# Optimization experiments

Hardware: AMD Instinct MI355X
Metric: run time of the kernel (lower is better)

The kernel has to match this reference:

```python
import jax, jax.numpy as jnp
import numpy as np

ALPHA = 0.2  # LeakyReLU slope
EPS = 1e-5   # LayerNorm eps (torch default)
NEG = -9e15  # pyGAT mask fill


def _lnorm(x, g, b):
    mu = x.mean(-1, keepdims=True)
    var = ((x - mu) ** 2).mean(-1, keepdims=True)
    return (x - mu) / jnp.sqrt(var + EPS) * g + b


def _gat_rel(h, adj, W, a1, a2):
    # Canonical dense GAT layer, vectorized over relations.
    # h [N,di], adj [R,N,N] int, W [R,di,do], a1/a2 [R,do]
    Wh = jnp.einsum('ni,rio->rno', h, W)                     # [R,N,do]
    f1 = jnp.einsum('rno,ro->rn', Wh, a1)
    f2 = jnp.einsum('rno,ro->rn', Wh, a2)
    e = jax.nn.leaky_relu(f1[:, :, None] + f2[:, None, :], ALPHA)  # [R,N,N]
    att = jax.nn.softmax(jnp.where(adj > 0, e, NEG), axis=-1)
    return jax.nn.elu(jnp.einsum('rnm,rmo->rno', att, Wh))   # [R,N,do]


def setup_inputs() -> dict:
    key = jax.random.key(0)
    N, D, R, Q, C = 2048, 512, 4, 32, 64
    HE, HD = 2, 2
    ks = jax.random.split(key, 16)
    s = 0.05
    return {
        'x': jax.random.normal(ks[0], (N, D), jnp.float32),
        'rel_adj': jax.random.randint(ks[1], (R, N, N), 0, 2, jnp.int32),
        'qembedding1': jax.random.normal(ks[2], (Q, D), jnp.float32),
        'qnode_idx': jax.random.randint(ks[3], (8,), 0, N, jnp.int32),
        'choices_nodes_idx': jax.random.randint(ks[4], (5, C), 0, N, jnp.int32),
        'Wc': jax.random.normal(ks[5], (D, D), jnp.float32) * s,
        'bc': jnp.zeros((D,), jnp.float32),
        'wq': jax.random.normal(ks[6], (D,), jnp.float32) * s,
        'enc_W': jax.random.normal(ks[7], (HE, R, D, D), jnp.float32) * s,
        'enc_a1': jax.random.normal(ks[8], (HE, R, D), jnp.float32) * s,
        'enc_a2': jax.random.normal(ks[9], (HE, R, D), jnp.float32) * s,
        'dec_W': jax.random.normal(ks[10], (HD, R, D, D), jnp.float32) * s,
        'dec_a1': jax.random.normal(ks[11], (HD, R, D), jnp.float32) * s,
        'dec_a2': jax.random.normal(ks[12], (HD, R, D), jnp.float32) * s,
        'ln_g': jnp.ones((D,), jnp.float32),
        'ln_b': jnp.zeros((D,), jnp.float32),
        'Wqc': jax.random.normal(ks[13], (D, D), jnp.float32) * s,
        'bqc': jnp.zeros((D,), jnp.float32),
        'Wout': jax.random.normal(ks[14], (D, 1), jnp.float32) * s,
        'bout': jnp.zeros((1,), jnp.float32),
    }


def reference(x, rel_adj, qembedding1, qnode_idx, choices_nodes_idx,
              Wc, bc, wq, enc_W, enc_a1, enc_a2, dec_W, dec_a1, dec_a2,
              ln_g, ln_b, Wqc, bqc, Wout, bout):
    # QuestionLayer: attention-pool the question token sequence -> [D]
    qemb = jax.nn.softmax(qembedding1 @ wq) @ qembedding1
    # question-gated node embeddings (Conv1d k=1 == linear over features)
    p = jax.nn.sigmoid((x @ Wc.T + bc) @ qemb)[:, None]       # [N,1]
    x = p * x + (1.0 - p) * qemb[None, :]
    # encoder: per-relation GAT + LayerNorm, maxpool over relations
    for h in range(enc_W.shape[0]):
        xr = _gat_rel(x, rel_adj, enc_W[h], enc_a1[h], enc_a2[h])
        x = _lnorm(xr, ln_g, ln_b).max(axis=0)                # [N,D]
    # decoder (transpose attentions): last round skips LayerNorm
    xd = x
    HD = dec_W.shape[0]
    for i in range(HD):
        xr = _gat_rel(xd, rel_adj, dec_W[i], dec_a1[i], dec_a2[i])
        if i < HD - 1:
            xr = _lnorm(xr, ln_g, ln_b)
        xd = xr.max(axis=0)
    # QuestionChoiceLayer over the 5 choices (all present -> mask gate = 1)
    cnodes = x[choices_nodes_idx]                             # [5,C,D]
    qproj = qembedding1.mean(axis=0) @ Wqc + bqc              # [D]
    scores = jax.nn.softmax(jnp.einsum('kcd,d->kc', cnodes, qproj), axis=-1)
    cembed = jnp.einsum('kc,kcd->kd', scores, cnodes)         # [5,D]
    cout = jax.nn.log_softmax(cembed @ Wout + bout, axis=0)   # [5,1]
    return cout, xd
```

## Files before the change

kernel.cpp:

```cpp
#include <hip/hip_runtime.h>
#include <hip/hip_bf16.h>

typedef __hip_bfloat16 bf16;
typedef __attribute__((ext_vector_type(8))) short bf16x8_t;
typedef __attribute__((ext_vector_type(4))) float f32x4_t;

#define N 2048
#define D 512
#define R 4
#define Q 32
#define NC 64
#define ALPHA 0.2f
#define LNEPS 1e-5f
#define NEGC -9e15f

__device__ __forceinline__ float ldf(const float* p) { return *p; }
__device__ __forceinline__ float ldf(const bf16* p) { return __bfloat162float(*p); }
__device__ __forceinline__ void stf(float* p, float v) { *p = v; }
__device__ __forceinline__ void stf(bf16* p, float v) { *p = __float2bfloat16(v); }

__device__ __forceinline__ short f2b(float f) {
    unsigned u = __builtin_bit_cast(unsigned, f);
    unsigned r = u + 0x7FFFu + ((u >> 16) & 1u);
    return (short)(r >> 16);
}
__device__ __forceinline__ float b2fs(short s) {
    unsigned u = ((unsigned)(unsigned short)s) << 16;
    return __builtin_bit_cast(float, u);
}
__device__ __forceinline__ unsigned pk2(float a, float b) {
    return (unsigned)(unsigned short)f2b(a) | (((unsigned)(unsigned short)f2b(b)) << 16);
}

__device__ __forceinline__ float waveReduceSum(float v) {
#pragma unroll
    for (int o = 32; o > 0; o >>= 1) v += __shfl_down(v, o, 64);
    return v;
}
__device__ __forceinline__ float waveReduceMax(float v) {
#pragma unroll
    for (int o = 32; o > 0; o >>= 1) v = fmaxf(v, __shfl_down(v, o, 64));
    return v;
}

__global__ __launch_bounds__(512) void k_prep(const float* __restrict__ qe1, const float* __restrict__ wq,
                                              const float* __restrict__ Wc, const float* __restrict__ bc,
                                              const float* __restrict__ Wqc, const float* __restrict__ bqc,
                                              float* __restrict__ qemb, float* __restrict__ vvec,
                                              float* __restrict__ qproj, float* __restrict__ c0) {
    __shared__ float logits[Q];
    __shared__ float sw[Q];
    __shared__ float meanq[D];
    __shared__ float qembs[D];
    __shared__ float red8[8];
    int tid = threadIdx.x;
    int wave = tid >> 6, lane = tid & 63;
    for (int q = wave; q < Q; q += 8) {
        float s = 0.f;
        for (int d = lane; d < D; d += 64) s += qe1[q * D + d] * wq[d];
        s = waveReduceSum(s);
        if (lane == 0) logits[q] = s;
    }
    __syncthreads();
    if (tid == 0) {
        float m = -3e38f;
        for (int q = 0; q < Q; q++) m = fmaxf(m, logits[q]);
        float ssum = 0.f;
        for (int q = 0; q < Q; q++) { float e = __expf(logits[q] - m); sw[q] = e; ssum += e; }
        float inv = 1.f / ssum;
        for (int q = 0; q < Q; q++) sw[q] *= inv;
    }
    __syncthreads();
    {
        float acc = 0.f, mq = 0.f;
#pragma unroll 4
        for (int q = 0; q < Q; q++) { float xv = qe1[q * D + tid]; acc += sw[q] * xv; mq += xv; }
        qembs[tid] = acc;
        meanq[tid] = mq * (1.f / Q);
        qemb[tid] = acc;
    }
    __syncthreads();
    {
        float v = 0.f, qp = 0.f;
        for (int i = 0; i < D; i++) {
            v = fmaf(qembs[i], Wc[i * D + tid], v);
            qp = fmaf(meanq[i], Wqc[i * D + tid], qp);
        }
        vvec[tid] = v;
        qproj[tid] = qp + bqc[tid];
    }
    float cc = qembs[tid] * bc[tid];
    cc = waveReduceSum(cc);
    if (lane == 0) red8[wave] = cc;
    __syncthreads();
    if (tid == 0) {
        float t = 0.f;
        for (int i = 0; i < 8; i++) t += red8[i];
        c0[0] = t;
    }
}

__global__ __launch_bounds__(256) void k_prepw(const float* __restrict__ W, short* __restrict__ Wt) {
    int mi = blockIdx.z;
    int k0 = blockIdx.y * 32, d0 = blockIdx.x * 32;
    __shared__ float L[32][33];
    int tid = threadIdx.x;
    const float* Wm = W + (size_t)mi * D * D;
    {
        int kr = tid >> 3, dc = (tid & 7) * 4;
        float4 f = *(const float4*)&Wm[(size_t)(k0 + kr) * D + d0 + dc];
        L[kr][dc] = f.x; L[kr][dc + 1] = f.y; L[kr][dc + 2] = f.z; L[kr][dc + 3] = f.w;
    }
    __syncthreads();
    short* Wo = Wt + (size_t)mi * D * D;
    {
        int dr = tid >> 3, kc = (tid & 7) * 4;
        uint2 o;
        o.x = pk2(L[kc][dr], L[kc + 1][dr]);
        o.y = pk2(L[kc + 2][dr], L[kc + 3][dr]);
        *(uint2*)&Wo[(size_t)(d0 + dr) * D + k0 + kc] = o;
    }
}

__global__ __launch_bounds__(256) void k_zero12(float* __restrict__ f1, float* __restrict__ f2) {
    int i = blockIdx.x * 256 + threadIdx.x;
    f1[i] = 0.f;
    f2[i] = 0.f;
}

__global__ __launch_bounds__(256) void k_gate(const float* __restrict__ x, const float* __restrict__ vvec,
                                              const float* __restrict__ qemb, const float* __restrict__ c0,
                                              bf16* __restrict__ xcur) {
    int n = blockIdx.x;
    int tid = threadIdx.x;
    __shared__ float red[4];
    __shared__ float ps;
    float x0 = x[n * D + tid], x1 = x[n * D + tid + 256];
    float v = x0 * vvec[tid] + x1 * vvec[tid + 256];
    v = waveReduceSum(v);
    if ((tid & 63) == 0) red[tid >> 6] = v;
    __syncthreads();
    if (tid == 0) {
        float dot = (red[0] + red[1]) + (red[2] + red[3]) + c0[0];
        ps = 1.f / (1.f + __expf(-dot));
    }
    __syncthreads();
    float p = ps;
    stf(&xcur[n * D + tid], p * x0 + (1.f - p) * qemb[tid]);
    stf(&xcur[n * D + tid + 256], p * x1 + (1.f - p) * qemb[tid + 256]);
}

__global__ __launch_bounds__(256) void k_gemm_mfma(const bf16* __restrict__ xin, const short* __restrict__ Wt,
                                                   short* __restrict__ WhT, const float* __restrict__ a1b,
                                                   const float* __restrict__ a2b, float* __restrict__ f1,
                                                   float* __restrict__ f2) {
    int r = blockIdx.z;
    int m0 = blockIdx.x * 64;
    int d0 = blockIdx.y * 64;
    int tid = threadIdx.x;
    int w = tid >> 6, l = tid & 63, g = l >> 4, rs = l & 15;
    int wn = w >> 1, wd = w & 1;
    __shared__ __align__(16) short Al[64 * 40];
    __shared__ __align__(16) short Bl[64 * 40];
    __shared__ __align__(16) short Tt[64 * 80];
    __shared__ float a1s[64], a2s[64];
    __shared__ float r1[4][64], r2[4][64];
    if (tid < 64) {
        a1s[tid] = a1b[r * D + d0 + tid];
        a2s[tid] = a2b[r * D + d0 + tid];
    }
    f32x4_t acc[2][2];
#pragma unroll
    for (int i = 0; i < 2; i++)
#pragma unroll
        for (int j = 0; j < 2; j++) acc[i][j] = (f32x4_t)(0.0f);

    const short* Wtr = Wt + (size_t)r * D * D;
    int sn = tid >> 2;
    int sk = (tid & 3) * 8;
    for (int k0 = 0; k0 < D; k0 += 32) {
        __syncthreads();
        {
            *(uint4*)&Al[sn * 40 + sk] = *(const uint4*)&xin[(size_t)(m0 + sn) * D + k0 + sk];
            *(uint4*)&Bl[sn * 40 + sk] = *(const uint4*)&Wtr[(size_t)(d0 + sn) * D + k0 + sk];
        }
        __syncthreads();
        union UA { bf16x8_t v; uint2 u[2]; };
        UA a[2], b;
#pragma unroll
        for (int nf = 0; nf < 2; nf++) {
            int arow = wn * 32 + nf * 16 + rs;
            a[nf].u[0] = *(const uint2*)&Al[arow * 40 + 4 * g];
            a[nf].u[1] = *(const uint2*)&Al[arow * 40 + 16 + 4 * g];
        }
#pragma unroll
        for (int df = 0; df < 2; df++) {
            int brow = wd * 32 + df * 16 + rs;
            b.u[0] = *(const uint2*)&Bl[brow * 40 + 4 * g];
            b.u[1] = *(const uint2*)&Bl[brow * 40 + 16 + 4 * g];
            acc[0][df] = __builtin_amdgcn_mfma_f32_16x16x32_bf16(a[0].v, b.v, acc[0][df], 0, 0, 0);
            acc[1][df] = __builtin_amdgcn_mfma_f32_16x16x32_bf16(a[1].v, b.v, acc[1][df], 0, 0, 0);
        }
    }
    __syncthreads();
#pragma unroll
    for (int nf = 0; nf < 2; nf++)
#pragma unroll
        for (int df = 0; df < 2; df++) {
            int nl = wn * 32 + nf * 16 + 4 * g;
            int dl = wd * 32 + df * 16 + rs;
            uint2 o;
            o.x = pk2(acc[nf][df][0], acc[nf][df][1]);
            o.y = pk2(acc[nf][df][2], acc[nf][df][3]);
            *(uint2*)&Tt[dl * 80 + nl] = o;
        }
    __syncthreads();
    {
        int dl = tid >> 2;
        int nc = (tid & 3) * 16;
        uint4 v0 = *(const uint4*)&Tt[dl * 80 + nc];
        uint4 v1 = *(const uint4*)&Tt[dl * 80 + nc + 8];
        short* op = WhT + ((size_t)r * D + d0 + dl) * N + m0 + nc;
        *(uint4*)op = v0;
        *(uint4*)(op + 8) = v1;
    }
    {
        int m = tid & 63, dg = tid >> 6;
        float s1 = 0.f, s2 = 0.f;
#pragma unroll
        for (int d = 0; d < 16; d++) {
            int dd = dg + d * 4;
            float wv = b2fs(Tt[dd * 80 + m]);
            s1 = fmaf(wv, a1s[dd], s1);
            s2 = fmaf(wv, a2s[dd], s2);
        }
        r1[dg][m] = s1;
        r2[dg][m] = s2;
    }
    __syncthreads();
    if (tid < 64) {
        float v1 = (r1[0][tid] + r1[1][tid]) + (r1[2][tid] + r1[3][tid]);
        float v2 = (r2[0][tid] + r2[1][tid]) + (r2[2][tid] + r2[3][tid]);
        atomicAdd(&f1[r * N + m0 + tid], v1);
        atomicAdd(&f2[r * N + m0 + tid], v2);
    }
}

__global__ __launch_bounds__(512) void k_pv_nm(const int* __restrict__ adj, const float* __restrict__ f1,
                                               const float* __restrict__ f2, const short* __restrict__ WhT,
                                               bf16* __restrict__ xr) {
    int r = blockIdx.y;
    int n0 = blockIdx.x * 32;
    int tid = threadIdx.x;
    int w = tid >> 6, l = tid & 63, g = l >> 4, rs = l & 15;
    __shared__ __align__(16) short Pl[2][32 * 40];
    __shared__ __align__(16) short Whl[2][512 * 40];
    __shared__ float sl[32], f1s[32];
    if (tid < 32) f1s[tid] = f1[r * N + n0 + tid];
    __syncthreads();
    f32x4_t acc[2][4];
#pragma unroll
    for (int i = 0; i < 2; i++)
#pragma unroll
        for (int j = 0; j < 4; j++) acc[i][j] = (f32x4_t)(0.0f);

    int pn = tid >> 3, pm4 = (tid & 7) * 4;
    const float* f2r = f2 + r * N;
    const int* arowb = adj + ((size_t)r * N + n0 + (pn & 31)) * N + pm4;
    int4 av;
    float4 fv;
    float f1v = 0.f;
    float myl = 0.f;
    int j = tid - 256;
    if (tid < 256) {
        f1v = f1s[pn];
        av = *(const int4*)(arowb);
        fv = *(const float4*)&f2r[pm4];
    }

    const int NT = N / 32;

#define PRODUCE(tt, bb)                                                                              \
    if (tid < 256) {                                                                                 \
        float t0 = f1v + fv.x; t0 = t0 >= 0.f ? t0 : ALPHA * t0;                                     \
        float t1 = f1v + fv.y; t1 = t1 >= 0.f ? t1 : ALPHA * t1;                                     \
        float t2 = f1v + fv.z; t2 = t2 >= 0.f ? t2 : ALPHA * t2;                                     \
        float t3 = f1v + fv.w; t3 = t3 >= 0.f ? t3 : ALPHA * t3;                                     \
        float e0 = (av.x > 0) ? __expf(fminf(t0, 60.f)) : 0.f;                                       \
        float e1 = (av.y > 0) ? __expf(fminf(t1, 60.f)) : 0.f;                                       \
        float e2 = (av.z > 0) ? __expf(fminf(t2, 60.f)) : 0.f;                                       \
        float e3 = (av.w > 0) ? __expf(fminf(t3, 60.f)) : 0.f;                                       \
        myl += (e0 + e1) + (e2 + e3);                                                                \
        uint2 pw;                                                                                    \
        pw.x = pk2(e0, e1);                                                                          \
        pw.y = pk2(e2, e3);                                                                          \
        *(uint2*)&Pl[bb][pn * 40 + pm4] = pw;                                                        \
        if ((tt) + 1 < NT) {                                                                         \
            av = *(const int4*)(arowb + ((tt) + 1) * 32);                                            \
            fv = *(const float4*)&f2r[((tt) + 1) * 32 + pm4];                                        \
        }                                                                                            \
    } else {                                                                                         \
        _Pragma("unroll") for (int i = 0; i < 8; i++) {                                              \
            int v = j + i * 256;                                                                     \
            int dd = v >> 2, mc = (v & 3) * 8;                                                       \
            *(uint4*)&Whl[bb][dd * 40 + mc] = *(const uint4*)&WhT[((size_t)r * D + dd) * N + (tt) * 32 + mc]; \
        }                                                                                            \
    }

    PRODUCE(0, 0);
    __syncthreads();

    for (int t = 0; t < NT; t++) {
        int cur = t & 1;
        if (t + 1 < NT) { PRODUCE(t + 1, (cur ^ 1)); }
        union UA { bf16x8_t v; uint2 u[2]; };
        UA a[2], b;
#pragma unroll
        for (int nf = 0; nf < 2; nf++) {
            int arow = nf * 16 + rs;
            a[nf].u[0] = *(const uint2*)&Pl[cur][arow * 40 + 4 * g];
            a[nf].u[1] = *(const uint2*)&Pl[cur][arow * 40 + 16 + 4 * g];
        }
#pragma unroll
        for (int df = 0; df < 4; df++) {
            int brow = w * 64 + df * 16 + rs;
            b.u[0] = *(const uint2*)&Whl[cur][brow * 40 + 4 * g];
            b.u[1] = *(const uint2*)&Whl[cur][brow * 40 + 16 + 4 * g];
            acc[0][df] = __builtin_amdgcn_mfma_f32_16x16x32_bf16(a[0].v, b.v, acc[0][df], 0, 0, 0);
            acc[1][df] = __builtin_amdgcn_mfma_f32_16x16x32_bf16(a[1].v, b.v, acc[1][df], 0, 0, 0);
        }
        __syncthreads();
    }
#undef PRODUCE
    if (tid < 256) {
        float v = myl;
#pragma unroll
        for (int msk = 1; msk < 8; msk <<= 1) v += __shfl_xor(v, msk, 8);
        if ((tid & 7) == 0) sl[pn] = v;
    }
    __syncthreads();
    float inv[2][4];
#pragma unroll
    for (int nf = 0; nf < 2; nf++)
#pragma unroll
        for (int reg = 0; reg < 4; reg++) inv[nf][reg] = 1.f / sl[nf * 16 + 4 * g + reg];
#pragma unroll
    for (int nf = 0; nf < 2; nf++)
#pragma unroll
        for (int df = 0; df < 4; df++)
#pragma unroll
            for (int reg = 0; reg < 4; reg++) {
                int n = n0 + nf * 16 + 4 * g + reg;
                int d = w * 64 + df * 16 + rs;
                float v = acc[nf][df][reg] * inv[nf][reg];
                v = v > 0.f ? v : (__expf(v) - 1.f);
                stf(&xr[((size_t)r * N + n) * D + d], v);
            }
}

__global__ __launch_bounds__(256) void k_lnmax(const bf16* __restrict__ xr, const float* __restrict__ g,
                                               const float* __restrict__ b, bf16* __restrict__ xout) {
    int n = blockIdx.x;
    int tid = threadIdx.x;
    int wave = tid >> 6, lane = tid & 63;
    __shared__ float redA[4], redB[4];
    float g0 = g[tid], g1 = g[tid + 256];
    float bb0 = b[tid], bb1 = b[tid + 256];
    float mx0 = -3e38f, mx1 = -3e38f;
    for (int r = 0; r < R; r++) {
        const bf16* row = xr + ((size_t)(r * N + n)) * D;
        float v0 = ldf(&row[tid]), v1 = ldf(&row[tid + 256]);
        float s = v0 + v1;
        float ss = fmaf(v0, v0, v1 * v1);
        s = waveReduceSum(s);
        ss = waveReduceSum(ss);
        if (lane == 0) { redA[wave] = s; redB[wave] = ss; }
        __syncthreads();
        float mu = ((redA[0] + redA[1]) + (redA[2] + redA[3])) * (1.f / D);
        float ex2 = ((redB[0] + redB[1]) + (redB[2] + redB[3])) * (1.f / D);
        float inv = 1.f / sqrtf(ex2 - mu * mu + LNEPS);
        mx0 = fmaxf(mx0, (v0 - mu) * inv * g0 + bb0);
        mx1 = fmaxf(mx1, (v1 - mu) * inv * g1 + bb1);
        __syncthreads();
    }
    stf(&xout[n * D + tid], mx0);
    stf(&xout[n * D + tid + 256], mx1);
}

__global__ __launch_bounds__(256) void k_maxout(const bf16* __restrict__ xr, float* __restrict__ out) {
    size_t idx = (size_t)blockIdx.x * 256 + threadIdx.x;
    float m = ldf(&xr[idx]);
    m = fmaxf(m, ldf(&xr[(size_t)N * D + idx]));
    m = fmaxf(m, ldf(&xr[2 * (size_t)N * D + idx]));
    m = fmaxf(m, ldf(&xr[3 * (size_t)N * D + idx]));
    out[idx] = m;
}

__global__ __launch_bounds__(256) void k_cscore(const bf16* __restrict__ xe, const int* __restrict__ cidx,
                                                const float* __restrict__ qproj, const float* __restrict__ Wout,
                                                float* __restrict__ scw, float* __restrict__ dvw) {
    int wv = threadIdx.x >> 6, lane = threadIdx.x & 63;
    int p = blockIdx.x * 4 + wv;
    const bf16* row = xe + (size_t)cidx[p] * D;
    float s1 = 0.f, s2 = 0.f;
#pragma unroll
    for (int i = 0; i < 8; i++) {
        int d = lane + i * 64;
        float v = ldf(&row[d]);
        s1 = fmaf(v, qproj[d], s1);
        s2 = fmaf(v, Wout[d], s2);
    }
    s1 = waveReduceSum(s1);
    s2 = waveReduceSum(s2);
    if (lane == 0) { scw[p] = s1; dvw[p] = s2; }
}

__global__ __launch_bounds__(64) void k_cfinal(const float* __restrict__ scw, const float* __restrict__ dvw,
                                               const float* __restrict__ bout, float* __restrict__ out) {
    int lane = threadIdx.x;
    __shared__ float lg[5];
    for (int k = 0; k < 5; k++) {
        float v = scw[k * NC + lane];
        float m = waveReduceMax(v);
        m = __shfl(m, 0, 64);
        float e = __expf(v - m);
        float s = waveReduceSum(e);
        s = __shfl(s, 0, 64);
        float t = (e / s) * dvw[k * NC + lane];
        t = waveReduceSum(t);
        if (lane == 0) lg[k] = t + bout[0];
    }
    __syncthreads();
    if (lane == 0) {
        float m = -3e38f;
        for (int k = 0; k < 5; k++) m = fmaxf(m, lg[k]);
        float s = 0.f;
        for (int k = 0; k < 5; k++) s += __expf(lg[k] - m);
        float lse = logf(s) + m;
        for (int k = 0; k < 5; k++) out[k] = lg[k] - lse;
    }
}

extern "C" void kernel_launch(void* const* d_in, const int* in_sizes, int n_in,
                              void* d_out, int out_size, void* d_ws, size_t ws_size,
                              hipStream_t stream) {
    bool skipQ = false;
    if (n_in > 4 && in_sizes[4] != 5 * NC && in_sizes[3] == 5 * NC) skipQ = true;
    auto IN = [&](int i) -> const void* {
        int j = (skipQ && i >= 4) ? i - 1 : i;
        return d_in[j];
    };
    const float* x = (const float*)IN(0);
    const int* adj = (const int*)IN(1);
    const float* qe1 = (const float*)IN(2);
    const int* cidx = (const int*)IN(4);
    const float* Wc = (const float*)IN(5);
    const float* bc = (const float*)IN(6);
    const float* wq = (const float*)IN(7);
    const float* encW = (const float*)IN(8);
    const float* enca1 = (const float*)IN(9);
    const float* enca2 = (const float*)IN(10);
    const float* decW = (const float*)IN(11);
    const float* deca1 = (const float*)IN(12);
    const float* deca2 = (const float*)IN(13);
    const float* lng = (const float*)IN(14);
    const float* lnb = (const float*)IN(15);
    const float* Wqc = (const float*)IN(16);
    const float* bqc = (const float*)IN(17);
    const float* Wout = (const float*)IN(18);
    const float* bout = (const float*)IN(19);
    float* out = (float*)d_out;

    char* w8 = (char*)d_ws;
    float* qemb = (float*)(w8 + 0);
    float* vvec = (float*)(w8 + 2048);
    float* qproj = (float*)(w8 + 4096);
    float* c0 = (float*)(w8 + 6144);
    float* f1 = (float*)(w8 + 8192);
    float* f2 = (float*)(w8 + 8192 + 32768);
    float* scw = (float*)(w8 + 8192 + 65536);
    float* dvw = (float*)(w8 + 8192 + 98304);
    const size_t ND = (size_t)N * D;
    bf16* xcur = (bf16*)(w8 + 139264);
    bf16* xd = (bf16*)(w8 + 139264 + ND * 2);
    short* WhT = (short*)(w8 + 139264 + ND * 4);
    bf16* xr = (bf16*)(w8 + 139264 + ND * 4 + R * ND * 2);
    short* Wt = (short*)xr;

    k_prep<<<1, 512, 0, stream>>>(qe1, wq, Wc, bc, Wqc, bqc, qemb, vvec, qproj, c0);
    k_gate<<<N, 256, 0, stream>>>(x, vvec, qemb, c0, xcur);

    for (int L = 0; L < 4; L++) {
        const float* Wb = (L < 2) ? encW + (size_t)L * R * D * D : decW + (size_t)(L - 2) * R * D * D;
        const float* a1 = (L < 2) ? enca1 + L * R * D : deca1 + (L - 2) * R * D;
        const float* a2 = (L < 2) ? enca2 + L * R * D : deca2 + (L - 2) * R * D;
        const bf16* xin = (L == 3) ? xd : xcur;
        k_prepw<<<dim3(16, 16, R), 256, 0, stream>>>(Wb, Wt);
        k_zero12<<<R * N / 256, 256, 0, stream>>>(f1, f2);
        k_gemm_mfma<<<dim3(N / 64, D / 64, R), 256, 0, stream>>>(xin, Wt, WhT, a1, a2, f1, f2);
        k_pv_nm<<<dim3(N / 32, R), 512, 0, stream>>>(adj, f1, f2, WhT, xr);
        if (L < 3)
            k_lnmax<<<N, 256, 0, stream>>>(xr, lng, lnb, (L < 2) ? xcur : xd);
        else
            k_maxout<<<N * D / 256, 256, 0, stream>>>(xr, out + 5);
    }
    k_cscore<<<80, 256, 0, stream>>>(xcur, cidx, qproj, Wout, scw, dvw);
    k_cfinal<<<1, 64, 0, stream>>>(scw, dvw, bout, out);
}
```

Measured before the change: 451.3 us.

## Restructure PV kernel pipeline with register prefetch and XCD-aware block mapping

The attention-times-Wh kernel now prefetches the WhT tile into registers one step ahead and the adjacency/f2 values two steps ahead, alternating two LDS buffers with one barrier per step. The goal is to hide global load latency behind the MFMA work. Blocks are launched as a flat 1D grid whose index is remapped so each XCD works on a single relation's WhT, which should improve L2 reuse. launch_bounds(512,2) asks for two blocks per CU, which caps registers per thread and risks spills given the extra prefetch registers.

```diff
diff --git a/kernel.cpp b/kernel.cpp
--- a/kernel.cpp
+++ b/kernel.cpp
@@ -246,11 +246,13 @@
     }
 }
 
-__global__ __launch_bounds__(512) void k_pv_nm(const int* __restrict__ adj, const float* __restrict__ f1,
-                                               const float* __restrict__ f2, const short* __restrict__ WhT,
-                                               bf16* __restrict__ xr) {
-    int r = blockIdx.y;
-    int n0 = blockIdx.x * 32;
+__global__ __launch_bounds__(512, 2) void k_pv_nm(const int* __restrict__ adj, const float* __restrict__ f1,
+                                                  const float* __restrict__ f2, const short* __restrict__ WhT,
+                                                  bf16* __restrict__ xr) {
+    int b = blockIdx.x;
+    int xcd = b & 7, idx = b >> 3;
+    int r = xcd & 3;
+    int n0 = ((xcd >> 2) * 32 + idx) * 32;
     int tid = threadIdx.x;
     int w = tid >> 6, l = tid & 63, g = l >> 4, rs = l & 15;
     __shared__ __align__(16) short Pl[2][32 * 40];
@@ -267,71 +269,76 @@
     int pn = tid >> 3, pm4 = (tid & 7) * 4;
     const float* f2r = f2 + r * N;
     const int* arowb = adj + ((size_t)r * N + n0 + (pn & 31)) * N + pm4;
-    int4 av;
-    float4 fv;
+    int4 avA, avB;
+    float4 fvA, fvB;
     float f1v = 0.f;
     float myl = 0.f;
-    int j = tid - 256;
+    int jd = (tid - 256) >> 2, jm = ((tid - 256) & 3) * 8;
+    uint4 wreg[8];
+    const int NT = N / 32;
+
     if (tid < 256) {
         f1v = f1s[pn];
-        av = *(const int4*)(arowb);
-        fv = *(const float4*)&f2r[pm4];
-    }
-
-    const int NT = N / 32;
-
-#define PRODUCE(tt, bb)                                                                              \
+        avA = *(const int4*)(arowb);
+        fvA = *(const float4*)&f2r[pm4];
+        avB = *(const int4*)(arowb + 32);
+        fvB = *(const float4*)&f2r[32 + pm4];
+    } else {
+#pragma unroll
+        for (int i = 0; i < 8; i++)
+            wreg[i] = *(const uint4*)&WhT[((size_t)r * D + jd + i * 64) * N + jm];
+    }
+
+#define PVITER(tt, cc, AV, FV)                                                                       \
     if (tid < 256) {                                                                                 \
-        float t0 = f1v + fv.x; t0 = t0 >= 0.f ? t0 : ALPHA * t0;                                     \
-        float t1 = f1v + fv.y; t1 = t1 >= 0.f ? t1 : ALPHA * t1;                                     \
-        float t2 = f1v + fv.z; t2 = t2 >= 0.f ? t2 : ALPHA * t2;                                     \
-        float t3 = f1v + fv.w; t3 = t3 >= 0.f ? t3 : ALPHA * t3;                                     \
-        float e0 = (av.x > 0) ? __expf(fminf(t0, 60.f)) : 0.f;                                       \
-        float e1 = (av.y > 0) ? __expf(fminf(t1, 60.f)) : 0.f;                                       \
-        float e2 = (av.z > 0) ? __expf(fminf(t2, 60.f)) : 0.f;                                       \
-        float e3 = (av.w > 0) ? __expf(fminf(t3, 60.f)) : 0.f;                                       \
+        float t0 = f1v + FV.x; t0 = t0 >= 0.f ? t0 : ALPHA * t0;                                     \
+        float t1 = f1v + FV.y; t1 = t1 >= 0.f ? t1 : ALPHA * t1;                                     \
+        float t2 = f1v + FV.z; t2 = t2 >= 0.f ? t2 : ALPHA * t2;                                     \
+        float t3 = f1v + FV.w; t3 = t3 >= 0.f ? t3 : ALPHA * t3;                                     \
+        float e0 = (AV.x > 0) ? __expf(fminf(t0, 60.f)) : 0.f;                                       \
+        float e1 = (AV.y > 0) ? __expf(fminf(t1, 60.f)) : 0.f;                                       \
+        float e2 = (AV.z > 0) ? __expf(fminf(t2, 60.f)) : 0.f;                                       \
+        float e3 = (AV.w > 0) ? __expf(fminf(t3, 60.f)) : 0.f;                                       \
         myl += (e0 + e1) + (e2 + e3);                                                                \
         uint2 pw;                                                                                    \
         pw.x = pk2(e0, e1);                                                                          \
         pw.y = pk2(e2, e3);                                                                          \
-        *(uint2*)&Pl[bb][pn * 40 + pm4] = pw;                                                        \
-        if ((tt) + 1 < NT) {                                                                         \
-            av = *(const int4*)(arowb + ((tt) + 1) * 32);                                            \
-            fv = *(const float4*)&f2r[((tt) + 1) * 32 + pm4];                                        \
+        *(uint2*)&Pl[cc][pn * 40 + pm4] = pw;                                                        \
+        if ((tt) + 2 < NT) {                                                                         \
+            AV = *(const int4*)(arowb + ((tt) + 2) * 32);                                            \
+            FV = *(const float4*)&f2r[((tt) + 2) * 32 + pm4];                                        \
         }                                                                                            \
     } else {                                                                                         \
-        _Pragma("unroll") for (int i = 0; i < 8; i++) {                                              \
-            int v = j + i * 256;                                                                     \
-            int dd = v >> 2, mc = (v & 3) * 8;                                                       \
-            *(uint4*)&Whl[bb][dd * 40 + mc] = *(const uint4*)&WhT[((size_t)r * D + dd) * N + (tt) * 32 + mc]; \
+        _Pragma("unroll") for (int i = 0; i < 8; i++)                                                \
+            *(uint4*)&Whl[cc][(jd + i * 64) * 40 + jm] = wreg[i];                                    \
+        if ((tt) + 1 < NT) {                                                                         \
+            _Pragma("unroll") for (int i = 0; i < 8; i++)                                            \
+                wreg[i] = *(const uint4*)&WhT[((size_t)r * D + jd + i * 64) * N + ((tt) + 1) * 32 + jm]; \
         }                                                                                            \
-    }
-
-    PRODUCE(0, 0);
-    __syncthreads();
-
-    for (int t = 0; t < NT; t++) {
-        int cur = t & 1;
-        if (t + 1 < NT) { PRODUCE(t + 1, (cur ^ 1)); }
-        union UA { bf16x8_t v; uint2 u[2]; };
-        UA a[2], b;
-#pragma unroll
-        for (int nf = 0; nf < 2; nf++) {
-            int arow = nf * 16 + rs;
-            a[nf].u[0] = *(const uint2*)&Pl[cur][arow * 40 + 4 * g];
-            a[nf].u[1] = *(const uint2*)&Pl[cur][arow * 40 + 16 + 4 * g];
-        }
-#pragma unroll
-        for (int df = 0; df < 4; df++) {
-            int brow = w * 64 + df * 16 + rs;
-            b.u[0] = *(const uint2*)&Whl[cur][brow * 40 + 4 * g];
-            b.u[1] = *(const uint2*)&Whl[cur][brow * 40 + 16 + 4 * g];
-            acc[0][df] = __builtin_amdgcn_mfma_f32_16x16x32_bf16(a[0].v, b.v, acc[0][df], 0, 0, 0);
-            acc[1][df] = __builtin_amdgcn_mfma_f32_16x16x32_bf16(a[1].v, b.v, acc[1][df], 0, 0, 0);
-        }
-        __syncthreads();
-    }
-#undef PRODUCE
+    }                                                                                                \
+    __syncthreads();                                                                                 \
+    {                                                                                                \
+        union UA { bf16x8_t v; uint2 u[2]; };                                                        \
+        UA a[2], bb;                                                                                 \
+        _Pragma("unroll") for (int nf = 0; nf < 2; nf++) {                                           \
+            int arow = nf * 16 + rs;                                                                 \
+            a[nf].u[0] = *(const uint2*)&Pl[cc][arow * 40 + 4 * g];                                  \
+            a[nf].u[1] = *(const uint2*)&Pl[cc][arow * 40 + 16 + 4 * g];                             \
+        }                                                                                            \
+        _Pragma("unroll") for (int df = 0; df < 4; df++) {                                           \
+            int brow = w * 64 + df * 16 + rs;                                                        \
+            bb.u[0] = *(const uint2*)&Whl[cc][brow * 40 + 4 * g];                                    \
+            bb.u[1] = *(const uint2*)&Whl[cc][brow * 40 + 16 + 4 * g];                               \
+            acc[0][df] = __builtin_amdgcn_mfma_f32_16x16x32_bf16(a[0].v, bb.v, acc[0][df], 0, 0, 0); \
+            acc[1][df] = __builtin_amdgcn_mfma_f32_16x16x32_bf16(a[1].v, bb.v, acc[1][df], 0, 0, 0); \
+        }                                                                                            \
+    }
+
+    for (int t = 0; t < NT; t += 2) {
+        PVITER(t, 0, avA, fvA);
+        PVITER(t + 1, 1, avB, fvB);
+    }
+#undef PVITER
     if (tid < 256) {
         float v = myl;
 #pragma unroll
@@ -498,7 +505,7 @@
         k_prepw<<<dim3(16, 16, R), 256, 0, stream>>>(Wb, Wt);
         k_zero12<<<R * N / 256, 256, 0, stream>>>(f1, f2);
         k_gemm_mfma<<<dim3(N / 64, D / 64, R), 256, 0, stream>>>(xin, Wt, WhT, a1, a2, f1, f2);
-        k_pv_nm<<<dim3(N / 32, R), 512, 0, stream>>>(adj, f1, f2, WhT, xr);
+        k_pv_nm<<<256, 512, 0, stream>>>(adj, f1, f2, WhT, xr);
         if (L < 3)
             k_lnmax<<<N, 256, 0, stream>>>(xr, lng, lnb, (L < 2) ? xcur : xd);
         else
```

Result: slower. 763.8 us (+69.2%).
